# Kernel tuning notes

Measured on AMD Instinct MI355X. Metric: run time of the kernel, lower is better.

The kernel has to match this reference:

```python
import jax, jax.numpy as jnp
import numpy as np

B, T, D = 2, 2048, 2048
H = 16
HD = D // H  # 128
THETA = 10000.0


def setup_inputs() -> dict:
    key = jax.random.key(0)
    kx, kq, ko = jax.random.split(key, 3)
    x = jax.random.normal(kx, (B, T, D), dtype=jnp.float32)
    # store weights pre-transposed: y = x @ W
    Wqkv = jax.random.normal(kq, (D, 3 * D), dtype=jnp.float32) * (D ** -0.5)
    Wout = jax.random.normal(ko, (D, D), dtype=jnp.float32) * (D ** -0.5)
    # rotary cache: [T, HD//2, 2] = (cos, sin)
    inv_freq = 1.0 / (THETA ** (jnp.arange(0, HD, 2, dtype=jnp.float32) / HD))
    angles = jnp.arange(T, dtype=jnp.float32)[:, None] * inv_freq[None, :]
    freqs_cis = jnp.stack([jnp.cos(angles), jnp.sin(angles)], axis=-1)
    return {"x": x, "Wqkv": Wqkv, "Wout": Wout, "freqs_cis": freqs_cis}


def _apply_rotary(freqs_cis, t):
    # t: [B, H, T, HD]; freqs_cis: [T, HD//2, 2]
    b, h, s, d = t.shape
    tr = t.reshape(b, h, s, d // 2, 2)
    cos = freqs_cis[:s, :, 0]  # [T, HD//2]
    sin = freqs_cis[:s, :, 1]
    x0, x1 = tr[..., 0], tr[..., 1]
    o0 = x0 * cos - x1 * sin
    o1 = x1 * cos + x0 * sin
    return jnp.stack([o0, o1], axis=-1).reshape(b, h, s, d)


def reference(x, Wqkv, Wout, freqs_cis):
    b, s, d = x.shape
    qkv = x @ Wqkv  # [B, T, 3D]
    # 'B T (three h d) -> B three h T d'
    qkv = qkv.reshape(b, s, 3, H, HD).transpose(0, 2, 3, 1, 4)
    q, k, v = qkv[:, 0], qkv[:, 1], qkv[:, 2]  # each [B, H, T, HD]
    q = _apply_rotary(freqs_cis, q)
    k = _apply_rotary(freqs_cis, k)
    # causal SDPA
    scale = 1.0 / jnp.sqrt(jnp.asarray(HD, dtype=q.dtype))
    scores = jnp.einsum('bhqd,bhkd->bhqk', q, k) * scale
    causal = jnp.tril(jnp.ones((s, s), dtype=bool))
    scores = jnp.where(causal, scores, jnp.finfo(scores.dtype).min)
    probs = jax.nn.softmax(scores, axis=-1)
    out = jnp.einsum('bhqk,bhkd->bhqd', probs, v)  # [B, H, T, HD]
    out = out.transpose(0, 2, 1, 3).reshape(b, s, d)  # 'B h T d -> B T (h d)'
    return out @ Wout
```

## Files before the change

### kernel.cpp

```cpp
#include <hip/hip_runtime.h>
#include <math.h>

#define B_   2
#define T_   2048
#define D_   2048
#define H_   16
#define HD_  128
#define QKV_LD 6144
#define SCALE 0.08838834764831845f

typedef __attribute__((ext_vector_type(4))) float f32x4;
typedef __attribute__((ext_vector_type(8))) short bf16x8;

static __device__ __forceinline__ unsigned short f2bf(float f) {
    unsigned u = __builtin_bit_cast(unsigned, f);
    return (unsigned short)((u + 0x7FFFu + ((u >> 16) & 1u)) >> 16);
}
static __device__ __forceinline__ float bf2f(unsigned short h) {
    unsigned u = ((unsigned)h) << 16;
    return __builtin_bit_cast(float, u);
}

__global__ __launch_bounds__(256)
void castx(const float* __restrict__ in, unsigned short* __restrict__ out) {
    size_t i = (size_t)blockIdx.x * 256 + threadIdx.x;
    const float4* p = (const float4*)in + 2 * i;
    float4 a = p[0], b = p[1];
    unsigned short tmp[8] = {f2bf(a.x), f2bf(a.y), f2bf(a.z), f2bf(a.w),
                             f2bf(b.x), f2bf(b.y), f2bf(b.z), f2bf(b.w)};
    ((uint4*)out)[i] = *(uint4*)tmp;
}

__global__ __launch_bounds__(256)
void wtrans(const float* __restrict__ W, unsigned short* __restrict__ Wt,
            int K, int N) {
    __shared__ float tile[64][65];
    int k0 = blockIdx.y * 64, n0 = blockIdx.x * 64;
    int t = threadIdx.x;
    #pragma unroll
    for (int i = 0; i < 4; ++i) {
        int f = t + 256 * i;
        int r = f >> 4, c4 = f & 15;
        float4 v = *(const float4*)(W + (size_t)(k0 + r) * N + n0 + c4 * 4);
        tile[r][c4 * 4 + 0] = v.x; tile[r][c4 * 4 + 1] = v.y;
        tile[r][c4 * 4 + 2] = v.z; tile[r][c4 * 4 + 3] = v.w;
    }
    __syncthreads();
    #pragma unroll
    for (int i = 0; i < 2; ++i) {
        int f = t + 256 * i;
        int r = f >> 3, c = f & 7;
        unsigned short tmp[8];
        #pragma unroll
        for (int j = 0; j < 8; ++j) tmp[j] = f2bf(tile[c * 8 + j][r]);
        *(uint4*)(Wt + (size_t)(n0 + r) * K + k0 + c * 8) = *(uint4*)tmp;
    }
}

template <bool OUT_BF16>
__global__ __launch_bounds__(256)
void gemm_bf16(const unsigned short* __restrict__ A,
               const unsigned short* __restrict__ Bt,
               float* __restrict__ Cf, unsigned short* __restrict__ Cb,
               int M, int N, int K) {
    __shared__ unsigned short As[128 * 64];
    __shared__ unsigned short Bs[128 * 64];
    int t = threadIdx.x;
    int wid = t >> 6, lane = t & 63;
    int wm = wid >> 1, wn = wid & 1;
    int lr = lane & 15, lg = lane >> 4;
    int m0 = blockIdx.y * 128, n0 = blockIdx.x * 128;

    f32x4 acc[4][4];
    #pragma unroll
    for (int a = 0; a < 4; ++a)
        #pragma unroll
        for (int b = 0; b < 4; ++b)
            acc[a][b] = (f32x4){0.f, 0.f, 0.f, 0.f};

    for (int k0 = 0; k0 < K; k0 += 64) {
        #pragma unroll
        for (int i = 0; i < 4; ++i) {
            int f = t + 256 * i;
            int row = f >> 3, ch = f & 7;
            uint4 v = *(const uint4*)(A + (size_t)(m0 + row) * K + k0 + ch * 8);
            *(uint4*)((char*)As + row * 128 + ((ch * 16) ^ ((row & 7) << 4))) = v;
        }
        #pragma unroll
        for (int i = 0; i < 4; ++i) {
            int f = t + 256 * i;
            int row = f >> 3, ch = f & 7;
            uint4 v = *(const uint4*)(Bt + (size_t)(n0 + row) * K + k0 + ch * 8);
            *(uint4*)((char*)Bs + row * 128 + ((ch * 16) ^ ((row & 7) << 4))) = v;
        }
        __syncthreads();
        #pragma unroll
        for (int ks = 0; ks < 2; ++ks) {
            bf16x8 af[4], bfm[4];
            #pragma unroll
            for (int mb = 0; mb < 4; ++mb) {
                int row = wm * 64 + mb * 16 + lr;
                af[mb] = *(const bf16x8*)((const char*)As + row * 128 +
                          (((ks * 32 + lg * 8) * 2) ^ ((row & 7) << 4)));
            }
            #pragma unroll
            for (int nb = 0; nb < 4; ++nb) {
                int row = wn * 64 + nb * 16 + lr;
                bfm[nb] = *(const bf16x8*)((const char*)Bs + row * 128 +
                           (((ks * 32 + lg * 8) * 2) ^ ((row & 7) << 4)));
            }
            #pragma unroll
            for (int mb = 0; mb < 4; ++mb)
                #pragma unroll
                for (int nb = 0; nb < 4; ++nb)
                    acc[mb][nb] = __builtin_amdgcn_mfma_f32_16x16x32_bf16(
                        af[mb], bfm[nb], acc[mb][nb], 0, 0, 0);
        }
        __syncthreads();
    }
    #pragma unroll
    for (int mb = 0; mb < 4; ++mb)
        #pragma unroll
        for (int nb = 0; nb < 4; ++nb)
            #pragma unroll
            for (int r = 0; r < 4; ++r) {
                int row = m0 + wm * 64 + mb * 16 + lg * 4 + r;
                int col = n0 + wn * 64 + nb * 16 + lr;
                if (OUT_BF16)
                    Cb[(size_t)row * N + col] = f2bf(acc[mb][nb][r]);
                else
                    Cf[(size_t)row * N + col] = acc[mb][nb][r];
            }
}

__global__ __launch_bounds__(256)
void rope_qk(unsigned short* __restrict__ qkvb, const float* __restrict__ fc) {
    int gid = blockIdx.x * 256 + threadIdx.x;
    int ch  = gid & 15;
    int h   = (gid >> 4) & 15;
    int sel = (gid >> 8) & 1;
    int row = gid >> 9;
    int t   = row & (T_ - 1);

    unsigned short* p = qkvb + (size_t)row * QKV_LD + sel * D_ + h * HD_ + ch * 8;
    uint4 v = *(uint4*)p;
    unsigned short* s = (unsigned short*)&v;
    const float* f = fc + ((size_t)t * 64 + ch * 4) * 2;
    float4 fA = *(const float4*)f;
    float4 fB = *(const float4*)(f + 4);
    float x0 = bf2f(s[0]), x1 = bf2f(s[1]), x2 = bf2f(s[2]), x3 = bf2f(s[3]);
    float x4 = bf2f(s[4]), x5 = bf2f(s[5]), x6 = bf2f(s[6]), x7 = bf2f(s[7]);
    unsigned short o[8];
    o[0] = f2bf(x0 * fA.x - x1 * fA.y);
    o[1] = f2bf(x1 * fA.x + x0 * fA.y);
    o[2] = f2bf(x2 * fA.z - x3 * fA.w);
    o[3] = f2bf(x3 * fA.z + x2 * fA.w);
    o[4] = f2bf(x4 * fB.x - x5 * fB.y);
    o[5] = f2bf(x5 * fB.x + x4 * fB.y);
    o[6] = f2bf(x6 * fB.z - x7 * fB.w);
    o[7] = f2bf(x7 * fB.z + x6 * fB.w);
    *(uint4*)p = *(uint4*)o;
}

__global__ __launch_bounds__(256)
void vT_build(const unsigned short* __restrict__ qkvb,
              unsigned short* __restrict__ vT) {
    __shared__ unsigned short tile[128][72];
    int t0 = blockIdx.x * 64;
    int bh = blockIdx.y;
    int b = bh >> 4, h = bh & 15;
    int tid = threadIdx.x;
    #pragma unroll
    for (int i = 0; i < 4; ++i) {
        int f = tid + 256 * i;
        int tr = f >> 4, ch = f & 15;
        uint4 v = *(const uint4*)(qkvb +
            (size_t)(b * T_ + t0 + tr) * QKV_LD + 2 * D_ + h * HD_ + ch * 8);
        unsigned short* s = (unsigned short*)&v;
        #pragma unroll
        for (int j = 0; j < 8; ++j) tile[ch * 8 + j][tr] = s[j];
    }
    __syncthreads();
    #pragma unroll
    for (int i = 0; i < 4; ++i) {
        int f = tid + 256 * i;
        int d = f >> 3, ch = f & 7;
        uint4 v = *(uint4*)(&tile[d][ch * 8]);
        *(uint4*)(vT + ((size_t)(bh * 128 + d)) * T_ + t0 + ch * 8) = v;
    }
}

__global__ __launch_bounds__(256)
void attn_mfma(const unsigned short* __restrict__ qkvb,
               const unsigned short* __restrict__ vT,
               unsigned short* __restrict__ attnb) {
    __shared__ unsigned short Qs[64 * 128];
    __shared__ unsigned short Ks[64 * 128];
    __shared__ unsigned short Vts[128 * 64];
    __shared__ unsigned short Ps[4 * 16 * 72];

    int t = threadIdx.x;
    int wid = t >> 6, lane = t & 63;
    int lr = lane & 15, lg = lane >> 4;
    int qt = (int)gridDim.x - 1 - (int)blockIdx.x;
    int bh = blockIdx.y;
    int b = bh >> 4, h = bh & 15;
    int qt0 = qt * 64;

    const unsigned short* qbase = qkvb + (size_t)(b * T_) * QKV_LD + h * HD_;
    const unsigned short* kbase = qbase + D_;
    const unsigned short* vbase = vT + (size_t)bh * 128 * T_;

    #pragma unroll
    for (int i = 0; i < 4; ++i) {
        int f = t + 256 * i;
        int row = f >> 4, ch = f & 15;
        uint4 v = *(const uint4*)(qbase + (size_t)(qt0 + row) * QKV_LD + ch * 8);
        *(uint4*)((char*)Qs + row * 256 + ((ch * 16) ^ ((row & 7) << 4))) = v;
    }

    f32x4 o[8];
    #pragma unroll
    for (int nb = 0; nb < 8; ++nb) o[nb] = (f32x4){0.f, 0.f, 0.f, 0.f};
    float m_r = -1e30f, l_r = 0.f;
    const int qrow_g = qt0 + wid * 16 + lr;

    for (int kt = 0; kt <= qt; ++kt) {
        #pragma unroll
        for (int i = 0; i < 4; ++i) {
            int f = t + 256 * i;
            int row = f >> 4, ch = f & 15;
            uint4 v = *(const uint4*)(kbase + (size_t)(kt * 64 + row) * QKV_LD + ch * 8);
            *(uint4*)((char*)Ks + row * 256 + ((ch * 16) ^ ((row & 7) << 4))) = v;
        }
        #pragma unroll
        for (int i = 0; i < 4; ++i) {
            int f = t + 256 * i;
            int row = f >> 3, ch = f & 7;
            uint4 v = *(const uint4*)(vbase + (size_t)row * T_ + kt * 64 + ch * 8);
            *(uint4*)((char*)Vts + row * 128 + ((ch * 16) ^ ((row & 7) << 4))) = v;
        }
        __syncthreads();

        f32x4 s[4];
        #pragma unroll
        for (int kb = 0; kb < 4; ++kb) s[kb] = (f32x4){0.f, 0.f, 0.f, 0.f};
        #pragma unroll
        for (int kd = 0; kd < 4; ++kd) {
            int qrow = wid * 16 + lr;
            bf16x8 qf = *(const bf16x8*)((const char*)Qs + qrow * 256 +
                         (((kd * 32 + lg * 8) * 2) ^ ((qrow & 7) << 4)));
            #pragma unroll
            for (int kb = 0; kb < 4; ++kb) {
                int krow = kb * 16 + lr;
                bf16x8 kf = *(const bf16x8*)((const char*)Ks + krow * 256 +
                             (((kd * 32 + lg * 8) * 2) ^ ((krow & 7) << 4)));
                s[kb] = __builtin_amdgcn_mfma_f32_16x16x32_bf16(kf, qf, s[kb], 0, 0, 0);
            }
        }

        float sv[4][4];
        bool diag = (kt == qt);
        #pragma unroll
        for (int kb = 0; kb < 4; ++kb)
            #pragma unroll
            for (int r = 0; r < 4; ++r) {
                float v = s[kb][r] * SCALE;
                int key_g = kt * 64 + kb * 16 + 4 * lg + r;
                if (diag && key_g > qrow_g) v = -1e30f;
                sv[kb][r] = v;
            }
        float mt = -1e30f;
        #pragma unroll
        for (int kb = 0; kb < 4; ++kb)
            #pragma unroll
            for (int r = 0; r < 4; ++r) mt = fmaxf(mt, sv[kb][r]);
        mt = fmaxf(mt, __shfl_xor(mt, 16));
        mt = fmaxf(mt, __shfl_xor(mt, 32));
        float mnew = fmaxf(m_r, mt);
        float alpha = __expf(m_r - mnew);
        float psum = 0.f;
        unsigned pw[4][2];
        #pragma unroll
        for (int kb = 0; kb < 4; ++kb) {
            float p0 = __expf(sv[kb][0] - mnew);
            float p1 = __expf(sv[kb][1] - mnew);
            float p2 = __expf(sv[kb][2] - mnew);
            float p3 = __expf(sv[kb][3] - mnew);
            psum += p0 + p1 + p2 + p3;
            pw[kb][0] = (unsigned)f2bf(p0) | ((unsigned)f2bf(p1) << 16);
            pw[kb][1] = (unsigned)f2bf(p2) | ((unsigned)f2bf(p3) << 16);
        }
        psum += __shfl_xor(psum, 16);
        psum += __shfl_xor(psum, 32);
        l_r = l_r * alpha + psum;
        m_r = mnew;

        float a0 = __shfl(alpha, 4 * lg + 0, 16);
        float a1 = __shfl(alpha, 4 * lg + 1, 16);
        float a2 = __shfl(alpha, 4 * lg + 2, 16);
        float a3 = __shfl(alpha, 4 * lg + 3, 16);
        #pragma unroll
        for (int nb = 0; nb < 8; ++nb) {
            o[nb][0] *= a0; o[nb][1] *= a1; o[nb][2] *= a2; o[nb][3] *= a3;
        }

        unsigned short* pbase = Ps + wid * 1152 + lr * 72;
        #pragma unroll
        for (int kb = 0; kb < 4; ++kb) {
            uint2 w; w.x = pw[kb][0]; w.y = pw[kb][1];
            *(uint2*)(pbase + kb * 16 + 4 * lg) = w;
        }
        #pragma unroll
        for (int ks = 0; ks < 2; ++ks) {
            bf16x8 pa = *(const bf16x8*)(pbase + ks * 32 + 8 * lg);
            #pragma unroll
            for (int nb = 0; nb < 8; ++nb) {
                int vrow = nb * 16 + lr;
                bf16x8 vf = *(const bf16x8*)((const char*)Vts + vrow * 128 +
                             (((ks * 32 + lg * 8) * 2) ^ ((vrow & 7) << 4)));
                o[nb] = __builtin_amdgcn_mfma_f32_16x16x32_bf16(pa, vf, o[nb], 0, 0, 0);
            }
        }
        __syncthreads();
    }

    float linv = 1.0f / l_r;
    float li0 = __shfl(linv, 4 * lg + 0, 16);
    float li1 = __shfl(linv, 4 * lg + 1, 16);
    float li2 = __shfl(linv, 4 * lg + 2, 16);
    float li3 = __shfl(linv, 4 * lg + 3, 16);
    #pragma unroll
    for (int nb = 0; nb < 8; ++nb) {
        float li[4] = {li0, li1, li2, li3};
        #pragma unroll
        for (int r = 0; r < 4; ++r) {
            int trow = qt0 + wid * 16 + 4 * lg + r;
            attnb[((size_t)(b * T_ + trow)) * D_ + h * HD_ + nb * 16 + lr] =
                f2bf(o[nb][r] * li[r]);
        }
    }
}

extern "C" void kernel_launch(void* const* d_in, const int* in_sizes, int n_in,
                              void* d_out, int out_size, void* d_ws, size_t ws_size,
                              hipStream_t stream) {
    const float* x    = (const float*)d_in[0];
    const float* Wqkv = (const float*)d_in[1];
    const float* Wout = (const float*)d_in[2];
    const float* fc   = (const float*)d_in[3];
    float* out = (float*)d_out;

    char* ws = (char*)d_ws;
    unsigned short* xb    = (unsigned short*)(ws);
    unsigned short* attnb = xb;
    unsigned short* WqkvT = (unsigned short*)(ws + 16777216);
    unsigned short* WoutT = (unsigned short*)(ws + 41943040);
    unsigned short* qkvb  = (unsigned short*)(ws + 50331648);
    unsigned short* vT    = (unsigned short*)(ws + 100663296);

    dim3 blk(256);

    castx<<<4096, blk, 0, stream>>>(x, xb);
    wtrans<<<dim3(96, 32), blk, 0, stream>>>(Wqkv, WqkvT, 2048, 6144);
    wtrans<<<dim3(32, 32), blk, 0, stream>>>(Wout, WoutT, 2048, 2048);

    gemm_bf16<true><<<dim3(48, 32), blk, 0, stream>>>(xb, WqkvT, nullptr, qkvb,
                                                      4096, 6144, 2048);
    rope_qk<<<8192, blk, 0, stream>>>(qkvb, fc);
    vT_build<<<dim3(32, 32), blk, 0, stream>>>(qkvb, vT);
    attn_mfma<<<dim3(32, 32), blk, 0, stream>>>(qkvb, vT, attnb);
    gemm_bf16<false><<<dim3(16, 32), blk, 0, stream>>>(attnb, WoutT, out, nullptr,
                                                       4096, 2048, 2048);
}
```

Measured before the change: 470.6 us.

## Use direct global-to-LDS loads, double-buffer attention K/V, remap workgroups, defer rescale

The GEMM and attention tile loads now use global_load_lds, which writes straight into swizzled LDS and skips the register round trip. The attention kernel double-buffers K/V so the next tile's load overlaps compute, keeps Q fragments in registers, and reuses the Q LDS buffer as P scratch. Both kernels get an XCD-aware workgroup index remap, and attention also raises wave priority around MFMA sections. A lazy online-softmax rescale skips the o/alpha update when the running max grows by at most 8. This risks correctness if the swizzle mapping of the direct LDS loads or the deferred max handling is wrong, and double-buffering raises LDS use, which can lower occupancy.

Result: faster. 424.2 us (-9.9%).

```diff
diff --git a/kernel.cpp b/kernel.cpp
--- a/kernel.cpp
+++ b/kernel.cpp
@@ -19,6 +19,12 @@
 static __device__ __forceinline__ float bf2f(unsigned short h) {
     unsigned u = ((unsigned)h) << 16;
     return __builtin_bit_cast(float, u);
+}
+
+static __device__ __forceinline__ void gload_lds16(const void* g, void* l) {
+    __builtin_amdgcn_global_load_lds(
+        (const __attribute__((address_space(1))) unsigned int*)g,
+        (__attribute__((address_space(3))) unsigned int*)l, 16, 0, 0);
 }
 
 __global__ __launch_bounds__(256)
@@ -69,7 +75,12 @@
     int wid = t >> 6, lane = t & 63;
     int wm = wid >> 1, wn = wid & 1;
     int lr = lane & 15, lg = lane >> 4;
-    int m0 = blockIdx.y * 128, n0 = blockIdx.x * 128;
+
+    int nwg = gridDim.x * gridDim.y;
+    int wg  = blockIdx.y * gridDim.x + blockIdx.x;
+    int wgs = (wg & 7) * (nwg >> 3) + (wg >> 3);
+    int m0 = (wgs / gridDim.x) * 128;
+    int n0 = (wgs % gridDim.x) * 128;
 
     f32x4 acc[4][4];
     #pragma unroll
@@ -81,17 +92,12 @@
     for (int k0 = 0; k0 < K; k0 += 64) {
         #pragma unroll
         for (int i = 0; i < 4; ++i) {
-            int f = t + 256 * i;
-            int row = f >> 3, ch = f & 7;
-            uint4 v = *(const uint4*)(A + (size_t)(m0 + row) * K + k0 + ch * 8);
-            *(uint4*)((char*)As + row * 128 + ((ch * 16) ^ ((row & 7) << 4))) = v;
-        }
-        #pragma unroll
-        for (int i = 0; i < 4; ++i) {
-            int f = t + 256 * i;
-            int row = f >> 3, ch = f & 7;
-            uint4 v = *(const uint4*)(Bt + (size_t)(n0 + row) * K + k0 + ch * 8);
-            *(uint4*)((char*)Bs + row * 128 + ((ch * 16) ^ ((row & 7) << 4))) = v;
+            int c = (wid * 4 + i) * 64 + lane;
+            int row = c >> 3, ch = (c & 7) ^ (row & 7);
+            gload_lds16(A + (size_t)(m0 + row) * K + k0 + ch * 8,
+                        (char*)As + (wid * 4 + i) * 1024);
+            gload_lds16(Bt + (size_t)(n0 + row) * K + k0 + ch * 8,
+                        (char*)Bs + (wid * 4 + i) * 1024);
         }
         __syncthreads();
         #pragma unroll
@@ -195,15 +201,17 @@
                const unsigned short* __restrict__ vT,
                unsigned short* __restrict__ attnb) {
     __shared__ unsigned short Qs[64 * 128];
-    __shared__ unsigned short Ks[64 * 128];
-    __shared__ unsigned short Vts[128 * 64];
-    __shared__ unsigned short Ps[4 * 16 * 72];
+    __shared__ unsigned short Ks[2][64 * 128];
+    __shared__ unsigned short Vts[2][128 * 64];
 
     int t = threadIdx.x;
     int wid = t >> 6, lane = t & 63;
     int lr = lane & 15, lg = lane >> 4;
-    int qt = (int)gridDim.x - 1 - (int)blockIdx.x;
-    int bh = blockIdx.y;
+
+    int wg  = blockIdx.x;
+    int wgs = (wg & 7) * 128 + (wg >> 3);
+    int bh  = wgs >> 5;
+    int qt  = 31 - (wgs & 31);
     int b = bh >> 4, h = bh & 15;
     int qt0 = qt * 64;
 
@@ -213,11 +221,33 @@
 
     #pragma unroll
     for (int i = 0; i < 4; ++i) {
-        int f = t + 256 * i;
-        int row = f >> 4, ch = f & 15;
-        uint4 v = *(const uint4*)(qbase + (size_t)(qt0 + row) * QKV_LD + ch * 8);
-        *(uint4*)((char*)Qs + row * 256 + ((ch * 16) ^ ((row & 7) << 4))) = v;
-    }
+        int c = (wid * 4 + i) * 64 + lane;
+        int row = c >> 4, ch = (c & 15) ^ (row & 7);
+        gload_lds16(qbase + (size_t)(qt0 + row) * QKV_LD + ch * 8,
+                    (char*)Qs + (wid * 4 + i) * 1024);
+    }
+    #pragma unroll
+    for (int i = 0; i < 4; ++i) {
+        int c = (wid * 4 + i) * 64 + lane;
+        int rowk = c >> 4, chk = (c & 15) ^ (rowk & 7);
+        gload_lds16(kbase + (size_t)rowk * QKV_LD + chk * 8,
+                    (char*)Ks[0] + (wid * 4 + i) * 1024);
+        int rowv = c >> 3, chv = (c & 7) ^ (rowv & 7);
+        gload_lds16(vbase + (size_t)rowv * T_ + chv * 8,
+                    (char*)Vts[0] + (wid * 4 + i) * 1024);
+    }
+    __syncthreads();
+
+    bf16x8 qf[4];
+    {
+        int qrow = wid * 16 + lr;
+        #pragma unroll
+        for (int kd = 0; kd < 4; ++kd)
+            qf[kd] = *(const bf16x8*)((const char*)Qs + qrow * 256 +
+                       (((kd * 32 + lg * 8) * 2) ^ ((qrow & 7) << 4)));
+    }
+    __syncthreads();
+    unsigned short* Ps = Qs;
 
     f32x4 o[8];
     #pragma unroll
@@ -226,38 +256,37 @@
     const int qrow_g = qt0 + wid * 16 + lr;
 
     for (int kt = 0; kt <= qt; ++kt) {
-        #pragma unroll
-        for (int i = 0; i < 4; ++i) {
-            int f = t + 256 * i;
-            int row = f >> 4, ch = f & 15;
-            uint4 v = *(const uint4*)(kbase + (size_t)(kt * 64 + row) * QKV_LD + ch * 8);
-            *(uint4*)((char*)Ks + row * 256 + ((ch * 16) ^ ((row & 7) << 4))) = v;
-        }
-        #pragma unroll
-        for (int i = 0; i < 4; ++i) {
-            int f = t + 256 * i;
-            int row = f >> 3, ch = f & 7;
-            uint4 v = *(const uint4*)(vbase + (size_t)row * T_ + kt * 64 + ch * 8);
-            *(uint4*)((char*)Vts + row * 128 + ((ch * 16) ^ ((row & 7) << 4))) = v;
-        }
-        __syncthreads();
+        int cur = kt & 1;
+        if (kt < qt) {
+            #pragma unroll
+            for (int i = 0; i < 4; ++i) {
+                int c = (wid * 4 + i) * 64 + lane;
+                int rowk = c >> 4, chk = (c & 15) ^ (rowk & 7);
+                gload_lds16(kbase + (size_t)((kt + 1) * 64 + rowk) * QKV_LD + chk * 8,
+                            (char*)Ks[cur ^ 1] + (wid * 4 + i) * 1024);
+                int rowv = c >> 3, chv = (c & 7) ^ (rowv & 7);
+                gload_lds16(vbase + (size_t)rowv * T_ + (kt + 1) * 64 + chv * 8,
+                            (char*)Vts[cur ^ 1] + (wid * 4 + i) * 1024);
+            }
+        }
+        const unsigned short* Kc = Ks[cur];
+        const unsigned short* Vc = Vts[cur];
 
         f32x4 s[4];
         #pragma unroll
         for (int kb = 0; kb < 4; ++kb) s[kb] = (f32x4){0.f, 0.f, 0.f, 0.f};
+        __builtin_amdgcn_s_setprio(1);
         #pragma unroll
         for (int kd = 0; kd < 4; ++kd) {
-            int qrow = wid * 16 + lr;
-            bf16x8 qf = *(const bf16x8*)((const char*)Qs + qrow * 256 +
-                         (((kd * 32 + lg * 8) * 2) ^ ((qrow & 7) << 4)));
             #pragma unroll
             for (int kb = 0; kb < 4; ++kb) {
                 int krow = kb * 16 + lr;
-                bf16x8 kf = *(const bf16x8*)((const char*)Ks + krow * 256 +
+                bf16x8 kf = *(const bf16x8*)((const char*)Kc + krow * 256 +
                              (((kd * 32 + lg * 8) * 2) ^ ((krow & 7) << 4)));
-                s[kb] = __builtin_amdgcn_mfma_f32_16x16x32_bf16(kf, qf, s[kb], 0, 0, 0);
-            }
-        }
+                s[kb] = __builtin_amdgcn_mfma_f32_16x16x32_bf16(kf, qf[kd], s[kb], 0, 0, 0);
+            }
+        }
+        __builtin_amdgcn_s_setprio(0);
 
         float sv[4][4];
         bool diag = (kt == qt);
@@ -277,8 +306,11 @@
             for (int r = 0; r < 4; ++r) mt = fmaxf(mt, sv[kb][r]);
         mt = fmaxf(mt, __shfl_xor(mt, 16));
         mt = fmaxf(mt, __shfl_xor(mt, 32));
-        float mnew = fmaxf(m_r, mt);
-        float alpha = __expf(m_r - mnew);
+
+        bool defer = __all(mt - m_r <= 8.0f) != 0;
+        float mnew  = defer ? m_r : fmaxf(m_r, mt);
+        float alpha = defer ? 1.0f : __expf(m_r - mnew);
+
         float psum = 0.f;
         unsigned pw[4][2];
         #pragma unroll
@@ -296,13 +328,15 @@
         l_r = l_r * alpha + psum;
         m_r = mnew;
 
-        float a0 = __shfl(alpha, 4 * lg + 0, 16);
-        float a1 = __shfl(alpha, 4 * lg + 1, 16);
-        float a2 = __shfl(alpha, 4 * lg + 2, 16);
-        float a3 = __shfl(alpha, 4 * lg + 3, 16);
-        #pragma unroll
-        for (int nb = 0; nb < 8; ++nb) {
-            o[nb][0] *= a0; o[nb][1] *= a1; o[nb][2] *= a2; o[nb][3] *= a3;
+        if (!defer) {
+            float a0 = __shfl(alpha, 4 * lg + 0, 16);
+            float a1 = __shfl(alpha, 4 * lg + 1, 16);
+            float a2 = __shfl(alpha, 4 * lg + 2, 16);
+            float a3 = __shfl(alpha, 4 * lg + 3, 16);
+            #pragma unroll
+            for (int nb = 0; nb < 8; ++nb) {
+                o[nb][0] *= a0; o[nb][1] *= a1; o[nb][2] *= a2; o[nb][3] *= a3;
+            }
         }
 
         unsigned short* pbase = Ps + wid * 1152 + lr * 72;
@@ -311,17 +345,19 @@
             uint2 w; w.x = pw[kb][0]; w.y = pw[kb][1];
             *(uint2*)(pbase + kb * 16 + 4 * lg) = w;
         }
+        __builtin_amdgcn_s_setprio(1);
         #pragma unroll
         for (int ks = 0; ks < 2; ++ks) {
             bf16x8 pa = *(const bf16x8*)(pbase + ks * 32 + 8 * lg);
             #pragma unroll
             for (int nb = 0; nb < 8; ++nb) {
                 int vrow = nb * 16 + lr;
-                bf16x8 vf = *(const bf16x8*)((const char*)Vts + vrow * 128 +
+                bf16x8 vf = *(const bf16x8*)((const char*)Vc + vrow * 128 +
                              (((ks * 32 + lg * 8) * 2) ^ ((vrow & 7) << 4)));
                 o[nb] = __builtin_amdgcn_mfma_f32_16x16x32_bf16(pa, vf, o[nb], 0, 0, 0);
             }
         }
+        __builtin_amdgcn_s_setprio(0);
         __syncthreads();
     }
 
@@ -369,7 +405,7 @@
                                                       4096, 6144, 2048);
     rope_qk<<<8192, blk, 0, stream>>>(qkvb, fc);
     vT_build<<<dim3(32, 32), blk, 0, stream>>>(qkvb, vT);
-    attn_mfma<<<dim3(32, 32), blk, 0, stream>>>(qkvb, vT, attnb);
+    attn_mfma<<<1024, blk, 0, stream>>>(qkvb, vT, attnb);
     gemm_bf16<false><<<dim3(16, 32), blk, 0, stream>>>(attnb, WoutT, out, nullptr,
                                                        4096, 2048, 2048);
 }
```
